# Optimization experiments

Measured on AMD Instinct MI355X. Metric: run time of the kernel, lower is better.

The kernel has to match this reference:

```python
import jax, jax.numpy as jnp
import numpy as np

BATCH, SEQ_LEN, N_FEATURES = 4096, 128, 32
# (input_size, hidden_size) for encoder_l1..l3, decoder_l1..l3
SIZES = [(N_FEATURES, 16), (16, 4), (4, 1), (1, 4), (4, 8), (8, 16)]
NAMES = ["e1", "e2", "e3", "d1", "d2", "d3"]


def setup_inputs() -> dict:
    key = jax.random.key(0)
    keys = jax.random.split(key, 27)
    inp = {"x": jax.random.normal(keys[0], (BATCH, SEQ_LEN, N_FEATURES), jnp.float32)}
    ki = 1
    for name, (din, h) in zip(NAMES, SIZES):
        s = 1.0 / np.sqrt(h)
        inp[name + "_Wih"] = jax.random.uniform(keys[ki], (4 * h, din), jnp.float32, -s, s); ki += 1
        inp[name + "_Whh"] = jax.random.uniform(keys[ki], (4 * h, h), jnp.float32, -s, s); ki += 1
        inp[name + "_bih"] = jax.random.uniform(keys[ki], (4 * h,), jnp.float32, -s, s); ki += 1
        inp[name + "_bhh"] = jax.random.uniform(keys[ki], (4 * h,), jnp.float32, -s, s); ki += 1
    s = 1.0 / np.sqrt(16)
    inp["Wout"] = jax.random.uniform(keys[25], (N_FEATURES, 16), jnp.float32, -s, s)
    inp["bout"] = jax.random.uniform(keys[26], (N_FEATURES,), jnp.float32, -s, s)
    return inp


def lstm(x, Wih, Whh, bih, bhh):
    """Single-layer batch_first LSTM, PyTorch gate order (i, f, g, o).
    x: [B, S, Din] -> [B, S, H] (h0 = c0 = 0)."""
    B = x.shape[0]
    H = Whh.shape[1]
    b = bih + bhh
    # Precompute input projections for all timesteps at once: [S, B, 4H]
    xg = jnp.einsum("bsd,gd->sbg", x, Wih) + b

    def step(carry, xg_t):
        h, c = carry
        gates = xg_t + h @ Whh.T  # [B, 4H]
        i, f, g, o = jnp.split(gates, 4, axis=-1)
        i = jax.nn.sigmoid(i)
        f = jax.nn.sigmoid(f)
        g = jnp.tanh(g)
        o = jax.nn.sigmoid(o)
        c = f * c + i * g
        h = o * jnp.tanh(c)
        return (h, c), h

    h0 = jnp.zeros((B, H), x.dtype)
    (_, _), hs = jax.lax.scan(step, (h0, h0), xg)
    return jnp.swapaxes(hs, 0, 1)  # [B, S, H]


def reference(x,
              e1_Wih, e1_Whh, e1_bih, e1_bhh,
              e2_Wih, e2_Whh, e2_bih, e2_bhh,
              e3_Wih, e3_Whh, e3_bih, e3_bhh,
              d1_Wih, d1_Whh, d1_bih, d1_bhh,
              d2_Wih, d2_Whh, d2_bih, d2_bhh,
              d3_Wih, d3_Whh, d3_bih, d3_bhh,
              Wout, bout):
    # Dropout layers are identity in eval mode.
    h = lstm(x, e1_Wih, e1_Whh, e1_bih, e1_bhh)
    h = lstm(h, e2_Wih, e2_Whh, e2_bih, e2_bhh)
    h = lstm(h, e3_Wih, e3_Whh, e3_bih, e3_bhh)
    enc = h[:, -1, :]                                   # [B, 1]
    h = jnp.broadcast_to(enc[:, None, :], (x.shape[0], SEQ_LEN, enc.shape[-1]))
    h = lstm(h, d1_Wih, d1_Whh, d1_bih, d1_bhh)
    h = lstm(h, d2_Wih, d2_Whh, d2_bih, d2_bhh)
    h = lstm(h, d3_Wih, d3_Whh, d3_bih, d3_bhh)
    return h @ Wout.T + bout                            # [B, S, n_features]
```

## Files before the change

kernel.cpp:

```cpp
#include <hip/hip_runtime.h>

#define LOG2E 1.44269504088896340736f

__device__ __forceinline__ float vexp2(float x){ float r; asm("v_exp_f32 %0, %1" : "=v"(r) : "v"(x)); return r; }
__device__ __forceinline__ float vrcp (float x){ float r; asm("v_rcp_f32 %0, %1" : "=v"(r) : "v"(x)); return r; }
template<int OFF> __device__ __forceinline__ float dsw(float v){
  return __int_as_float(__builtin_amdgcn_ds_swizzle(__float_as_int(v), OFF));
}
#define SWX(m)  dsw<((m)<<10)|0x1F>
#define BC16(k) dsw<((k)<<5)|0x10>
__device__ __forceinline__ float sigm(float x){ return vrcp(1.0f + vexp2(x * (-LOG2E))); }
__device__ __forceinline__ float tanh_f(float x){
  float s = vrcp(1.0f + vexp2(x * (-2.0f*LOG2E)));
  return s + s - 1.0f;
}

__global__ void __launch_bounds__(256)
lstm_ae_fused(const float* __restrict__ x,
              const float* __restrict__ e1Wi, const float* __restrict__ e1Wh, const float* __restrict__ e1bi, const float* __restrict__ e1bh,
              const float* __restrict__ e2Wi, const float* __restrict__ e2Wh, const float* __restrict__ e2bi, const float* __restrict__ e2bh,
              const float* __restrict__ e3Wi, const float* __restrict__ e3Wh, const float* __restrict__ e3bi, const float* __restrict__ e3bh,
              const float* __restrict__ d1Wi, const float* __restrict__ d1Wh, const float* __restrict__ d1bi, const float* __restrict__ d1bh,
              const float* __restrict__ d2Wi, const float* __restrict__ d2Wh, const float* __restrict__ d2bi, const float* __restrict__ d2bh,
              const float* __restrict__ d3Wi, const float* __restrict__ d3Wh, const float* __restrict__ d3bi, const float* __restrict__ d3bh,
              const float* __restrict__ Wout, const float* __restrict__ bout,
              float* __restrict__ out)
{
  const int tid  = threadIdx.x;
  const int lane = tid & 63;
  const int wv   = tid >> 6;
  const int gw   = blockIdx.x*4 + wv;
  const int bA   = gw*2, bB = gw*2 + 1;
  const float* __restrict__ xbA = x + (size_t)bA * 4096;
  const float* __restrict__ xbB = x + (size_t)bB * 4096;
  float* __restrict__ obA = out + (size_t)bA * 4096;
  float* __restrict__ obB = out + (size_t)bB * 4096;

  __shared__ float s_e1[13*64*4];
  __shared__ float s_e2[16*20];
  __shared__ float s_eb2[16];
  __shared__ float s_e3[4*8];
  __shared__ float s_d1[16*8];
  __shared__ float s_d2[32*20];
  __shared__ float s_d3[7*64*4];
  __shared__ float s_wo[32*20];
  __shared__ float s_x [4][512];
  __shared__ float s_h1[4][64];
  __shared__ float s_g1[4][64];
  __shared__ float s_g2[4][64];
  __shared__ float s_g3[4][64];

  if (tid < 64){
    const int l = tid;
    const float A1l = (l>=32 && l<48) ? 2.f : 1.f;
    for (int k=0;k<32;++k) s_e1[((k>>2)*64+l)*4+(k&3)]      = e1Wi[l*32+k]*A1l;
    for (int k=0;k<16;++k) s_e1[(((k>>2)+8)*64+l)*4+(k&3)]  = e1Wh[l*16+k]*A1l;
    s_e1[(12*64+l)*4] = (e1bi[l]+e1bh[l])*A1l;
    for (int k=0;k<8;++k)  s_d3[((k>>2)*64+l)*4+(k&3)]      = d3Wi[l*8+k]*A1l;
    for (int k=0;k<16;++k) s_d3[(((k>>2)+2)*64+l)*4+(k&3)]  = d3Wh[l*16+k]*A1l;
    s_d3[(6*64+l)*4] = (d3bi[l]+d3bh[l])*A1l;
    if (l < 16){
      const float A2l = (l>=8 && l<12) ? 2.f : 1.f;
      for (int k=0;k<16;++k) s_e2[l*20+k]    = e2Wi[l*16+k]*A2l;
      for (int k=0;k<4;++k)  s_e2[l*20+16+k] = e2Wh[l*4+k]*A2l;
      s_eb2[l] = (e2bi[l]+e2bh[l])*A2l;
      for (int k=0;k<4;++k)  s_d1[l*8+k] = d1Wh[l*4+k]*A2l;
      s_d1[l*8+4] = d1Wi[l]*A2l;
      s_d1[l*8+5] = (d1bi[l]+d1bh[l])*A2l;
    }
    if (l < 4){
      const float A3l = (l==2) ? 2.f : 1.f;
      for (int k=0;k<4;++k) s_e3[l*8+k] = e3Wi[l*4+k]*A3l;
      s_e3[l*8+4] = e3Wh[l]*A3l;
      s_e3[l*8+5] = (e3bi[l]+e3bh[l])*A3l;
    }
    if (l < 32){
      const float AD2l = (l>=16 && l<24) ? 2.f : 1.f;
      for (int k=0;k<4;++k) s_d2[l*20+k]   = d2Wi[l*4+k]*AD2l;
      for (int k=0;k<8;++k) s_d2[l*20+4+k] = d2Wh[l*8+k]*AD2l;
      s_d2[l*20+12] = (d2bi[l]+d2bh[l])*AD2l;
      for (int k=0;k<16;++k) s_wo[l*20+k] = Wout[l*16+k];
      s_wo[l*20+16] = bout[l];
    }
  }
  __syncthreads();

  const bool isg1 = (lane >= 32) && (lane < 48);
  const bool isg2 = ((lane & 15) >= 8) && ((lane & 15) < 12);
  const bool isg3 = ((lane & 3) == 2);
  const bool isgD2= ((lane & 31) >= 16) && ((lane & 31) < 24);
  const float A1 = isg1 ? 2.f : 1.f,  B1 = isg1 ? -1.f : 0.f;
  const float A2 = isg2 ? 2.f : 1.f,  B2 = isg2 ? -1.f : 0.f;
  const float A3 = isg3 ? 2.f : 1.f,  B3 = isg3 ? -1.f : 0.f;
  const float AD2= isgD2? 2.f : 1.f,  BD2= isgD2? -1.f : 0.f;
  const bool selA = ((lane & 16) == 0);
  const int  h16  = lane & 16;
  const int  h32  = lane & 32;
  const int  h32s = (lane & 32) >> 1;

  const float4* e1v = (const float4*)s_e1;
  const float4* d3v = (const float4*)s_d3;
  const float* r2  = &s_e2[(lane&15)*20];
  const float* r3  = &s_e3[(lane&3)*8];
  const float* rd1 = &s_d1[(lane&15)*8];
  const float* rd2 = &s_d2[(lane&31)*20];
  const float* rw  = &s_wo[(lane&31)*20];

  float h3b = 0.f;

  {
    float4 w1q[8], wh1q[4];
    #pragma unroll
    for (int g=0; g<8; ++g) w1q[g] = e1v[g*64+lane];
    #pragma unroll
    for (int g=0; g<4; ++g) wh1q[g] = e1v[(8+g)*64+lane];
    const float eb1 = s_e1[(12*64+lane)*4];
    float4 w2q0 = *(const float4*)(r2);
    float4 w2q1 = *(const float4*)(r2+4);
    float4 w2q2 = *(const float4*)(r2+8);
    float4 w2q3 = *(const float4*)(r2+12);
    float4 w2q4 = *(const float4*)(r2+16);
    const float eb2 = s_eb2[lane&15];
    float4 w30 = *(const float4*)(r3);
    const float w3h = r3[4], eb3 = r3[5];

    s_h1[wv][lane] = 0.f;
    float c1 = 0.f, c2 = 0.f, c3 = 0.f;
    float bc2_0 = 0.f, bc2_1 = 0.f, bc2_2 = 0.f, bc2_3 = 0.f;

    float4 pfA = ((const float4*)xbA)[lane];
    float4 pfB = ((const float4*)xbB)[lane];
    float xga[8], xgb[8];

    auto stage_and_xg = [&](int tc){
      ((float4*)&s_x[wv][0])[lane]   = pfA;
      ((float4*)&s_x[wv][256])[lane] = pfB;
      if (tc + 8 < 128){
        pfA = ((const float4*)(xbA + (tc+8)*32))[lane];
        pfB = ((const float4*)(xbB + (tc+8)*32))[lane];
      }
      #pragma unroll
      for (int tt=0; tt<8; ++tt){
        const float4* xA4 = (const float4*)&s_x[wv][tt*32];
        const float4* xB4 = (const float4*)&s_x[wv][256+tt*32];
        float pa0=eb1, pa1=0.f, pa2=0.f, pa3=0.f;
        float pb0=eb1, pb1=0.f, pb2=0.f, pb3=0.f;
        #pragma unroll
        for (int g=0; g<8; ++g){
          float4 w = w1q[g];
          float4 xa = xA4[g], xb = xB4[g];
          pa0 = fmaf(w.x, xa.x, pa0);  pb0 = fmaf(w.x, xb.x, pb0);
          pa1 = fmaf(w.y, xa.y, pa1);  pb1 = fmaf(w.y, xb.y, pb1);
          pa2 = fmaf(w.z, xa.z, pa2);  pb2 = fmaf(w.z, xb.z, pb2);
          pa3 = fmaf(w.w, xa.w, pa3);  pb3 = fmaf(w.w, xb.w, pb3);
        }
        xga[tt] = (pa0+pa1)+(pa2+pa3);
        xgb[tt] = (pb0+pb1)+(pb2+pb3);
      }
    };

    auto enc_iter = [&](int D1_, int D2_, int D3_, float xa, float xb){
      float4 ha0,ha1,ha2,ha3,hb0,hb1,hb2,hb3,qq0,qq1,qq2,qq3;
      float h1new = 0.f, nb0=0.f, nb1=0.f, nb2=0.f, nb3=0.f;
      if (D1_){
        const float4* h1A = (const float4*)&s_h1[wv][0];
        const float4* h1B = (const float4*)&s_h1[wv][16];
        ha0=h1A[0]; ha1=h1A[1]; ha2=h1A[2]; ha3=h1A[3];
        hb0=h1B[0]; hb1=h1B[1]; hb2=h1B[2]; hb3=h1B[3];
      }
      if (D2_){
        const float4* h1s = (const float4*)&s_h1[wv][h16];
        qq0=h1s[0]; qq1=h1s[1]; qq2=h1s[2]; qq3=h1s[3];
      }
      if (D1_){
        float aA0 = xa, aA1=0.f, aA2=0.f, aA3=0.f;
        float aB0 = xb, aB1=0.f, aB2=0.f, aB3=0.f;
        aA0=fmaf(wh1q[0].x,ha0.x,aA0); aB0=fmaf(wh1q[0].x,hb0.x,aB0);
        aA1=fmaf(wh1q[0].y,ha0.y,aA1); aB1=fmaf(wh1q[0].y,hb0.y,aB1);
        aA2=fmaf(wh1q[0].z,ha0.z,aA2); aB2=fmaf(wh1q[0].z,hb0.z,aB2);
        aA3=fmaf(wh1q[0].w,ha0.w,aA3); aB3=fmaf(wh1q[0].w,hb0.w,aB3);
        aA0=fmaf(wh1q[1].x,ha1.x,aA0); aB0=fmaf(wh1q[1].x,hb1.x,aB0);
        aA1=fmaf(wh1q[1].y,ha1.y,aA1); aB1=fmaf(wh1q[1].y,hb1.y,aB1);
        aA2=fmaf(wh1q[1].z,ha1.z,aA2); aB2=fmaf(wh1q[1].z,hb1.z,aB2);
        aA3=fmaf(wh1q[1].w,ha1.w,aA3); aB3=fmaf(wh1q[1].w,hb1.w,aB3);
        aA0=fmaf(wh1q[2].x,ha2.x,aA0); aB0=fmaf(wh1q[2].x,hb2.x,aB0);
        aA1=fmaf(wh1q[2].y,ha2.y,aA1); aB1=fmaf(wh1q[2].y,hb2.y,aB1);
        aA2=fmaf(wh1q[2].z,ha2.z,aA2); aB2=fmaf(wh1q[2].z,hb2.z,aB2);
        aA3=fmaf(wh1q[2].w,ha2.w,aA3); aB3=fmaf(wh1q[2].w,hb2.w,aB3);
        aA0=fmaf(wh1q[3].x,ha3.x,aA0); aB0=fmaf(wh1q[3].x,hb3.x,aB0);
        aA1=fmaf(wh1q[3].y,ha3.y,aA1); aB1=fmaf(wh1q[3].y,hb3.y,aB1);
        aA2=fmaf(wh1q[3].z,ha3.z,aA2); aB2=fmaf(wh1q[3].z,hb3.z,aB2);
        aA3=fmaf(wh1q[3].w,ha3.w,aA3); aB3=fmaf(wh1q[3].w,hb3.w,aB3);
        float vA = fmaf(sigm((aA0+aA1)+(aA2+aA3)), A1, B1);
        float vB = fmaf(sigm((aB0+aB1)+(aB2+aB3)), A1, B1);
        float t1A = SWX(16)(vA);
        float t2A = __shfl_xor(vA, 32, 64);
        float t3A = SWX(16)(t2A);
        float t1B = SWX(16)(vB);
        float t2B = __shfl_xor(vB, 32, 64);
        float t3B = SWX(16)(t2B);
        float ip = selA ? vA  : t1B;
        float fp = selA ? t1A : vB;
        float gp = selA ? t2A : t3B;
        float op = selA ? t3A : t2B;
        c1 = fmaf(fp, c1, ip*gp);
        h1new = op * tanh_f(c1);
      }
      if (D2_){
        float a0 = eb2, a1 = 0.f;
        a0 = fmaf(w2q0.x,qq0.x,a0);  a1 = fmaf(w2q0.y,qq0.y,a1);
        a0 = fmaf(w2q0.z,qq0.z,a0);  a1 = fmaf(w2q0.w,qq0.w,a1);
        a0 = fmaf(w2q1.x,qq1.x,a0);  a1 = fmaf(w2q1.y,qq1.y,a1);
        a0 = fmaf(w2q1.z,qq1.z,a0);  a1 = fmaf(w2q1.w,qq1.w,a1);
        a0 = fmaf(w2q2.x,qq2.x,a0);  a1 = fmaf(w2q2.y,qq2.y,a1);
        a0 = fmaf(w2q2.z,qq2.z,a0);  a1 = fmaf(w2q2.w,qq2.w,a1);
        a0 = fmaf(w2q3.x,qq3.x,a0);  a1 = fmaf(w2q3.y,qq3.y,a1);
        a0 = fmaf(w2q3.z,qq3.z,a0);  a1 = fmaf(w2q3.w,qq3.w,a1);
        a0 = fmaf(w2q4.x,bc2_0,a0);  a1 = fmaf(w2q4.y,bc2_1,a1);
        a0 = fmaf(w2q4.z,bc2_2,a0);  a1 = fmaf(w2q4.w,bc2_3,a1);
        float v2 = fmaf(sigm(a0+a1), A2, B2);
        float f2 = SWX(4)(v2), g2 = SWX(8)(v2), o2 = SWX(12)(v2);
        c2 = fmaf(f2, c2, v2*g2);
        float h2v = o2 * tanh_f(c2);
        nb0 = BC16(0)(h2v); nb1 = BC16(1)(h2v);
        nb2 = BC16(2)(h2v); nb3 = BC16(3)(h2v);
      }
      if (D3_){
        float a = fmaf(w3h, h3b, eb3);
        a = fmaf(w30.x, bc2_0, a);
        a = fmaf(w30.y, bc2_1, a);
        a = fmaf(w30.z, bc2_2, a);
        a = fmaf(w30.w, bc2_3, a);
        float v3 = fmaf(sigm(a), A3, B3);
        float f3 = SWX(1)(v3), g3 = SWX(2)(v3), o3 = SWX(3)(v3);
        c3 = fmaf(f3, c3, v3*g3);
        h3b = BC16(0)(o3 * tanh_f(c3));
      }
      if (D1_) s_h1[wv][lane] = h1new;
      if (D2_){ bc2_0 = nb0; bc2_1 = nb1; bc2_2 = nb2; bc2_3 = nb3; }
    };

    stage_and_xg(0);
    enc_iter(1,0,0, xga[0], xgb[0]);
    enc_iter(1,1,0, xga[1], xgb[1]);
    #pragma unroll
    for (int tt=2; tt<8; ++tt) enc_iter(1,1,1, xga[tt], xgb[tt]);
    for (int tc=8; tc<128; tc+=8){
      stage_and_xg(tc);
      #pragma unroll
      for (int tt=0; tt<8; ++tt) enc_iter(1,1,1, xga[tt], xgb[tt]);
    }
    enc_iter(0,1,1, 0.f, 0.f);
    enc_iter(0,0,1, 0.f, 0.f);
  }

  {
    const float encv = h3b;
    const float p1  = fmaf(rd1[4], encv, rd1[5]);
    const float bd2 = rd2[12];
    const float bd3 = s_d3[(6*64+lane)*4];
    const float bo  = rw[16];
    float4 wd1 = *(const float4*)(rd1);
    float4 w2a = *(const float4*)(rd2);
    float4 w2b = *(const float4*)(rd2+4);
    float4 w2c = *(const float4*)(rd2+8);
    float4 d3q[6];
    #pragma unroll
    for (int g=0; g<6; ++g) d3q[g] = d3v[g*64+lane];
    float4 woa = *(const float4*)(rw);
    float4 wob = *(const float4*)(rw+4);
    float4 woc = *(const float4*)(rw+8);
    float4 wod = *(const float4*)(rw+12);

    s_g1[wv][lane] = 0.f;  s_g2[wv][lane] = 0.f;  s_g3[wv][lane] = 0.f;
    float dc1 = 0.f, dc2 = 0.f, dc3 = 0.f;
    float* __restrict__ obSel = (lane < 32) ? (obA + lane) : (obB + lane - 32);

    auto dec_iter = [&](int D1_, int D2_, int D3_, int DL_, int TO){
      float4 g1q, g1s, g2a, g2b, p2a0, p2a1, p2b0, p2b1;
      float4 r3a0,r3a1,r3a2,r3a3, r3b0,r3b1,r3b2,r3b3, u0,u1,u2,u3;
      float g1new=0.f, g2new=0.f, g3new=0.f, ovv=0.f;
      if (D1_) g1q = *(const float4*)&s_g1[wv][h16];
      if (D2_){
        g1s = *(const float4*)&s_g1[wv][h32s];
        g2a = *(const float4*)&s_g2[wv][h32];
        g2b = *(const float4*)&s_g2[wv][h32+4];
      }
      if (D3_){
        const float4* g2A = (const float4*)&s_g2[wv][0];
        const float4* g2B = (const float4*)&s_g2[wv][32];
        p2a0=g2A[0]; p2a1=g2A[1]; p2b0=g2B[0]; p2b1=g2B[1];
        const float4* g3A = (const float4*)&s_g3[wv][0];
        const float4* g3B = (const float4*)&s_g3[wv][16];
        r3a0=g3A[0]; r3a1=g3A[1]; r3a2=g3A[2]; r3a3=g3A[3];
        r3b0=g3B[0]; r3b1=g3B[1]; r3b2=g3B[2]; r3b3=g3B[3];
      }
      if (DL_){
        const float4* g3s = (const float4*)&s_g3[wv][h32s];
        u0=g3s[0]; u1=g3s[1]; u2=g3s[2]; u3=g3s[3];
      }
      if (D1_){
        float a0 = p1, a1 = 0.f;
        a0 = fmaf(wd1.x, g1q.x, a0); a1 = fmaf(wd1.y, g1q.y, a1);
        a0 = fmaf(wd1.z, g1q.z, a0); a1 = fmaf(wd1.w, g1q.w, a1);
        float v1 = fmaf(sigm(a0+a1), A2, B2);
        float f1 = SWX(4)(v1), gg1 = SWX(8)(v1), o1 = SWX(12)(v1);
        dc1 = fmaf(f1, dc1, v1*gg1);
        g1new = o1 * tanh_f(dc1);
      }
      if (D2_){
        float a0 = bd2, a1 = 0.f;
        a0 = fmaf(w2a.x, g1s.x, a0); a1 = fmaf(w2a.y, g1s.y, a1);
        a0 = fmaf(w2a.z, g1s.z, a0); a1 = fmaf(w2a.w, g1s.w, a1);
        a0 = fmaf(w2b.x, g2a.x, a0); a1 = fmaf(w2b.y, g2a.y, a1);
        a0 = fmaf(w2b.z, g2a.z, a0); a1 = fmaf(w2b.w, g2a.w, a1);
        a0 = fmaf(w2c.x, g2b.x, a0); a1 = fmaf(w2c.y, g2b.y, a1);
        a0 = fmaf(w2c.z, g2b.z, a0); a1 = fmaf(w2c.w, g2b.w, a1);
        float v2 = fmaf(sigm(a0+a1), AD2, BD2);
        float f2 = SWX(8)(v2), gg2 = SWX(16)(v2), o2 = SWX(24)(v2);
        dc2 = fmaf(f2, dc2, v2*gg2);
        g2new = o2 * tanh_f(dc2);
      }
      if (D3_){
        float aA0=bd3, aA1=0.f, aA2=0.f, aA3=0.f;
        float aB0=bd3, aB1=0.f, aB2=0.f, aB3=0.f;
        aA0=fmaf(d3q[0].x,p2a0.x,aA0); aB0=fmaf(d3q[0].x,p2b0.x,aB0);
        aA1=fmaf(d3q[0].y,p2a0.y,aA1); aB1=fmaf(d3q[0].y,p2b0.y,aB1);
        aA2=fmaf(d3q[0].z,p2a0.z,aA2); aB2=fmaf(d3q[0].z,p2b0.z,aB2);
        aA3=fmaf(d3q[0].w,p2a0.w,aA3); aB3=fmaf(d3q[0].w,p2b0.w,aB3);
        aA0=fmaf(d3q[1].x,p2a1.x,aA0); aB0=fmaf(d3q[1].x,p2b1.x,aB0);
        aA1=fmaf(d3q[1].y,p2a1.y,aA1); aB1=fmaf(d3q[1].y,p2b1.y,aB1);
        aA2=fmaf(d3q[1].z,p2a1.z,aA2); aB2=fmaf(d3q[1].z,p2b1.z,aB2);
        aA3=fmaf(d3q[1].w,p2a1.w,aA3); aB3=fmaf(d3q[1].w,p2b1.w,aB3);
        aA0=fmaf(d3q[2].x,r3a0.x,aA0); aB0=fmaf(d3q[2].x,r3b0.x,aB0);
        aA1=fmaf(d3q[2].y,r3a0.y,aA1); aB1=fmaf(d3q[2].y,r3b0.y,aB1);
        aA2=fmaf(d3q[2].z,r3a0.z,aA2); aB2=fmaf(d3q[2].z,r3b0.z,aB2);
        aA3=fmaf(d3q[2].w,r3a0.w,aA3); aB3=fmaf(d3q[2].w,r3b0.w,aB3);
        aA0=fmaf(d3q[3].x,r3a1.x,aA0); aB0=fmaf(d3q[3].x,r3b1.x,aB0);
        aA1=fmaf(d3q[3].y,r3a1.y,aA1); aB1=fmaf(d3q[3].y,r3b1.y,aB1);
        aA2=fmaf(d3q[3].z,r3a1.z,aA2); aB2=fmaf(d3q[3].z,r3b1.z,aB2);
        aA3=fmaf(d3q[3].w,r3a1.w,aA3); aB3=fmaf(d3q[3].w,r3b1.w,aB3);
        aA0=fmaf(d3q[4].x,r3a2.x,aA0); aB0=fmaf(d3q[4].x,r3b2.x,aB0);
        aA1=fmaf(d3q[4].y,r3a2.y,aA1); aB1=fmaf(d3q[4].y,r3b2.y,aB1);
        aA2=fmaf(d3q[4].z,r3a2.z,aA2); aB2=fmaf(d3q[4].z,r3b2.z,aB2);
        aA3=fmaf(d3q[4].w,r3a2.w,aA3); aB3=fmaf(d3q[4].w,r3b2.w,aB3);
        aA0=fmaf(d3q[5].x,r3a3.x,aA0); aB0=fmaf(d3q[5].x,r3b3.x,aB0);
        aA1=fmaf(d3q[5].y,r3a3.y,aA1); aB1=fmaf(d3q[5].y,r3b3.y,aB1);
        aA2=fmaf(d3q[5].z,r3a3.z,aA2); aB2=fmaf(d3q[5].z,r3b3.z,aB2);
        aA3=fmaf(d3q[5].w,r3a3.w,aA3); aB3=fmaf(d3q[5].w,r3b3.w,aB3);
        float vA = fmaf(sigm((aA0+aA1)+(aA2+aA3)), A1, B1);
        float vB = fmaf(sigm((aB0+aB1)+(aB2+aB3)), A1, B1);
        float t1A = SWX(16)(vA);
        float t2A = __shfl_xor(vA, 32, 64);
        float t3A = SWX(16)(t2A);
        float t1B = SWX(16)(vB);
        float t2B = __shfl_xor(vB, 32, 64);
        float t3B = SWX(16)(t2B);
        float ip = selA ? vA  : t1B;
        float fp = selA ? t1A : vB;
        float gp = selA ? t2A : t3B;
        float op = selA ? t3A : t2B;
        dc3 = fmaf(fp, dc3, ip*gp);
        g3new = op * tanh_f(dc3);
      }
      if (DL_){
        float ov0 = bo, ov1 = 0.f;
        ov0 = fmaf(woa.x, u0.x, ov0);  ov1 = fmaf(woa.y, u0.y, ov1);
        ov0 = fmaf(woa.z, u0.z, ov0);  ov1 = fmaf(woa.w, u0.w, ov1);
        ov0 = fmaf(wob.x, u1.x, ov0);  ov1 = fmaf(wob.y, u1.y, ov1);
        ov0 = fmaf(wob.z, u1.z, ov0);  ov1 = fmaf(wob.w, u1.w, ov1);
        ov0 = fmaf(woc.x, u2.x, ov0);  ov1 = fmaf(woc.y, u2.y, ov1);
        ov0 = fmaf(woc.z, u2.z, ov0);  ov1 = fmaf(woc.w, u2.w, ov1);
        ov0 = fmaf(wod.x, u3.x, ov0);  ov1 = fmaf(wod.y, u3.y, ov1);
        ov0 = fmaf(wod.z, u3.z, ov0);  ov1 = fmaf(wod.w, u3.w, ov1);
        ovv = ov0 + ov1;
      }
      if (D1_) s_g1[wv][lane] = g1new;
      if (D2_) s_g2[wv][lane] = g2new;
      if (D3_) s_g3[wv][lane] = g3new;
      if (DL_) obSel[TO*32] = ovv;
    };

    dec_iter(1,0,0,0, 0);
    dec_iter(1,1,0,0, 0);
    dec_iter(1,1,1,0, 0);
    #pragma unroll 2
    for (int i=3; i<128; ++i) dec_iter(1,1,1,1, i-3);
    dec_iter(0,1,1,1, 125);
    dec_iter(0,0,1,1, 126);
    dec_iter(0,0,0,1, 127);
  }
}

extern "C" void kernel_launch(void* const* d_in, const int* in_sizes, int n_in,
                              void* d_out, int out_size, void* d_ws, size_t ws_size,
                              hipStream_t stream) {
  (void)in_sizes; (void)n_in; (void)d_ws; (void)ws_size; (void)out_size;
  const float* x    = (const float*)d_in[0];
  const float* e1Wi = (const float*)d_in[1];
  const float* e1Wh = (const float*)d_in[2];
  const float* e1bi = (const float*)d_in[3];
  const float* e1bh = (const float*)d_in[4];
  const float* e2Wi = (const float*)d_in[5];
  const float* e2Wh = (const float*)d_in[6];
  const float* e2bi = (const float*)d_in[7];
  const float* e2bh = (const float*)d_in[8];
  const float* e3Wi = (const float*)d_in[9];
  const float* e3Wh = (const float*)d_in[10];
  const float* e3bi = (const float*)d_in[11];
  const float* e3bh = (const float*)d_in[12];
  const float* d1Wi = (const float*)d_in[13];
  const float* d1Wh = (const float*)d_in[14];
  const float* d1bi = (const float*)d_in[15];
  const float* d1bh = (const float*)d_in[16];
  const float* d2Wi = (const float*)d_in[17];
  const float* d2Wh = (const float*)d_in[18];
  const float* d2bi = (const float*)d_in[19];
  const float* d2bh = (const float*)d_in[20];
  const float* d3Wi = (const float*)d_in[21];
  const float* d3Wh = (const float*)d_in[22];
  const float* d3bi = (const float*)d_in[23];
  const float* d3bh = (const float*)d_in[24];
  const float* Wout = (const float*)d_in[25];
  const float* boutp= (const float*)d_in[26];
  float* out = (float*)d_out;

  lstm_ae_fused<<<512, 256, 0, stream>>>(x,
      e1Wi, e1Wh, e1bi, e1bh,
      e2Wi, e2Wh, e2bi, e2bh,
      e3Wi, e3Wh, e3bi, e3bh,
      d1Wi, d1Wh, d1bi, d1bh,
      d2Wi, d2Wh, d2bi, d2bh,
      d3Wi, d3Wh, d3bi, d3bh,
      Wout, boutp, out);
}
```

Baseline: 196.7 us.

## Double-buffer x staging and interleave input projections with recurrent steps

The encoder's layer-1 input projection for the next 8-timestep chunk is now computed one step at a time, interleaved with the current chunk's recurrent iterations, using a double-buffered shared x tile. The aim is to fill the latency of the serial recurrence (transcendentals, swizzles) with independent FMA work instead of running the projection as a separate burst. The gate exchange also swaps a dependent two-swizzle chain for one direct xor-48 shuffle, shortening the critical path. This costs extra registers for the next chunk's projections and doubles the shared x buffer, which may lower occupancy.

Result: slower. 320.8 us (+63.1%).

```diff
diff --git a/kernel.cpp b/kernel.cpp
--- a/kernel.cpp
+++ b/kernel.cpp
@@ -44,7 +44,7 @@
   __shared__ float s_d2[32*20];
   __shared__ float s_d3[7*64*4];
   __shared__ float s_wo[32*20];
-  __shared__ float s_x [4][512];
+  __shared__ float s_x [4][2][512];
   __shared__ float s_h1[4][64];
   __shared__ float s_g1[4][64];
   __shared__ float s_g2[4][64];
@@ -128,35 +128,24 @@
     float c1 = 0.f, c2 = 0.f, c3 = 0.f;
     float bc2_0 = 0.f, bc2_1 = 0.f, bc2_2 = 0.f, bc2_3 = 0.f;
 
-    float4 pfA = ((const float4*)xbA)[lane];
-    float4 pfB = ((const float4*)xbB)[lane];
-    float xga[8], xgb[8];
-
-    auto stage_and_xg = [&](int tc){
-      ((float4*)&s_x[wv][0])[lane]   = pfA;
-      ((float4*)&s_x[wv][256])[lane] = pfB;
-      if (tc + 8 < 128){
-        pfA = ((const float4*)(xbA + (tc+8)*32))[lane];
-        pfB = ((const float4*)(xbB + (tc+8)*32))[lane];
-      }
+    float xga[8], xgb[8], nga[8], ngb[8];
+
+    auto xg_step = [&](int buf, int tt, float &oa, float &ob){
+      const float4* xA4 = (const float4*)&s_x[wv][buf][tt*32];
+      const float4* xB4 = (const float4*)&s_x[wv][buf][256+tt*32];
+      float pa0=eb1, pa1=0.f, pa2=0.f, pa3=0.f;
+      float pb0=eb1, pb1=0.f, pb2=0.f, pb3=0.f;
       #pragma unroll
-      for (int tt=0; tt<8; ++tt){
-        const float4* xA4 = (const float4*)&s_x[wv][tt*32];
-        const float4* xB4 = (const float4*)&s_x[wv][256+tt*32];
-        float pa0=eb1, pa1=0.f, pa2=0.f, pa3=0.f;
-        float pb0=eb1, pb1=0.f, pb2=0.f, pb3=0.f;
-        #pragma unroll
-        for (int g=0; g<8; ++g){
-          float4 w = w1q[g];
-          float4 xa = xA4[g], xb = xB4[g];
-          pa0 = fmaf(w.x, xa.x, pa0);  pb0 = fmaf(w.x, xb.x, pb0);
-          pa1 = fmaf(w.y, xa.y, pa1);  pb1 = fmaf(w.y, xb.y, pb1);
-          pa2 = fmaf(w.z, xa.z, pa2);  pb2 = fmaf(w.z, xb.z, pb2);
-          pa3 = fmaf(w.w, xa.w, pa3);  pb3 = fmaf(w.w, xb.w, pb3);
-        }
-        xga[tt] = (pa0+pa1)+(pa2+pa3);
-        xgb[tt] = (pb0+pb1)+(pb2+pb3);
-      }
+      for (int g=0; g<8; ++g){
+        float4 w = w1q[g];
+        float4 xa = xA4[g], xb = xB4[g];
+        pa0 = fmaf(w.x, xa.x, pa0);  pb0 = fmaf(w.x, xb.x, pb0);
+        pa1 = fmaf(w.y, xa.y, pa1);  pb1 = fmaf(w.y, xb.y, pb1);
+        pa2 = fmaf(w.z, xa.z, pa2);  pb2 = fmaf(w.z, xb.z, pb2);
+        pa3 = fmaf(w.w, xa.w, pa3);  pb3 = fmaf(w.w, xb.w, pb3);
+      }
+      oa = (pa0+pa1)+(pa2+pa3);
+      ob = (pb0+pb1)+(pb2+pb3);
     };
 
     auto enc_iter = [&](int D1_, int D2_, int D3_, float xa, float xb){
@@ -195,10 +184,10 @@
         float vB = fmaf(sigm((aB0+aB1)+(aB2+aB3)), A1, B1);
         float t1A = SWX(16)(vA);
         float t2A = __shfl_xor(vA, 32, 64);
-        float t3A = SWX(16)(t2A);
+        float t3A = __shfl_xor(vA, 48, 64);
         float t1B = SWX(16)(vB);
         float t2B = __shfl_xor(vB, 32, 64);
-        float t3B = SWX(16)(t2B);
+        float t3B = __shfl_xor(vB, 48, 64);
         float ip = selA ? vA  : t1B;
         float fp = selA ? t1A : vB;
         float gp = selA ? t2A : t3B;
@@ -240,15 +229,46 @@
       if (D2_){ bc2_0 = nb0; bc2_1 = nb1; bc2_2 = nb2; bc2_3 = nb3; }
     };
 
-    stage_and_xg(0);
-    enc_iter(1,0,0, xga[0], xgb[0]);
-    enc_iter(1,1,0, xga[1], xgb[1]);
+    float4 pfA = ((const float4*)xbA)[lane];
+    float4 pfB = ((const float4*)xbB)[lane];
+    ((float4*)&s_x[wv][0][0])[lane]   = pfA;
+    ((float4*)&s_x[wv][0][256])[lane] = pfB;
+    pfA = ((const float4*)(xbA + 8*32))[lane];
+    pfB = ((const float4*)(xbB + 8*32))[lane];
     #pragma unroll
-    for (int tt=2; tt<8; ++tt) enc_iter(1,1,1, xga[tt], xgb[tt]);
-    for (int tc=8; tc<128; tc+=8){
-      stage_and_xg(tc);
-      #pragma unroll
-      for (int tt=0; tt<8; ++tt) enc_iter(1,1,1, xga[tt], xgb[tt]);
+    for (int tt=0; tt<8; ++tt) xg_step(0, tt, xga[tt], xgb[tt]);
+
+    for (int c=0; c<16; ++c){
+      const int nb = (c+1)&1;
+      if (c < 15){
+        ((float4*)&s_x[wv][nb][0])[lane]   = pfA;
+        ((float4*)&s_x[wv][nb][256])[lane] = pfB;
+        if (c < 14){
+          pfA = ((const float4*)(xbA + (c+2)*8*32))[lane];
+          pfB = ((const float4*)(xbB + (c+2)*8*32))[lane];
+        }
+      }
+      if (c == 0){
+        enc_iter(1,0,0, xga[0], xgb[0]);
+        if (c < 15) xg_step(nb, 0, nga[0], ngb[0]);
+        enc_iter(1,1,0, xga[1], xgb[1]);
+        if (c < 15) xg_step(nb, 1, nga[1], ngb[1]);
+        #pragma unroll
+        for (int tt=2; tt<8; ++tt){
+          enc_iter(1,1,1, xga[tt], xgb[tt]);
+          if (c < 15) xg_step(nb, tt, nga[tt], ngb[tt]);
+        }
+      } else {
+        #pragma unroll
+        for (int tt=0; tt<8; ++tt){
+          enc_iter(1,1,1, xga[tt], xgb[tt]);
+          if (c < 15) xg_step(nb, tt, nga[tt], ngb[tt]);
+        }
+      }
+      if (c < 15){
+        #pragma unroll
+        for (int tt=0; tt<8; ++tt){ xga[tt] = nga[tt]; xgb[tt] = ngb[tt]; }
+      }
     }
     enc_iter(0,1,1, 0.f, 0.f);
     enc_iter(0,0,1, 0.f, 0.f);
@@ -352,10 +372,10 @@
         float vB = fmaf(sigm((aB0+aB1)+(aB2+aB3)), A1, B1);
         float t1A = SWX(16)(vA);
         float t2A = __shfl_xor(vA, 32, 64);
-        float t3A = SWX(16)(t2A);
+        float t3A = __shfl_xor(vA, 48, 64);
         float t1B = SWX(16)(vB);
         float t2B = __shfl_xor(vB, 32, 64);
-        float t3B = SWX(16)(t2B);
+        float t3B = __shfl_xor(vB, 48, 64);
         float ip = selA ? vA  : t1B;
         float fp = selA ? t1A : vB;
         float gp = selA ? t2A : t3B;
```
